# Kernel optimization log

Measured on AMD Instinct MI355X. Metric: run time of the kernel, lower is better.

The kernel has to match this reference:

```python
import jax, jax.numpy as jnp
import numpy as np

N_HEADS = 16
NEG_INF = -1e9


def setup_inputs() -> dict:
    key = jax.random.key(0)
    ks = jax.random.split(key, 8)
    B, S, D = 2, 2048, 1024
    HD = D // N_HEADS
    x = jax.random.normal(ks[0], (B, S, D), dtype=jnp.float32)
    # RoPE frequencies (llama-style): theta = 10000^(-2i/head_dim)
    inv_freq = 1.0 / (10000.0 ** (np.arange(0, HD, 2, dtype=np.float32) / HD))  # [HD//2]
    angles = np.arange(S, dtype=np.float32)[:, None] * inv_freq[None, :]        # [S, HD//2]
    freqs_cos = jnp.asarray(np.cos(angles))
    freqs_sin = jnp.asarray(np.sin(angles))
    # additive causal mask [1,1,S,S]
    mask = jnp.where(np.tril(np.ones((S, S), dtype=bool)), 0.0, NEG_INF).astype(jnp.float32)[None, None]
    scale = 0.02
    wq = jax.random.normal(ks[1], (D, D), dtype=jnp.float32) * scale
    wk = jax.random.normal(ks[2], (D, D), dtype=jnp.float32) * scale
    wv = jax.random.normal(ks[3], (D, D), dtype=jnp.float32) * scale
    wo = jax.random.normal(ks[4], (D, D), dtype=jnp.float32) * scale
    return {"x": x, "freqs_cos": freqs_cos, "freqs_sin": freqs_sin, "mask": mask,
            "wq": wq, "wk": wk, "wv": wv, "wo": wo}


def _rope(t, cos, sin):
    # t: [B,S,H,HD]; cos/sin: [S,HD//2]; complex mult (t0 + i t1) * (cos + i sin)
    b, s, h, hd = t.shape
    tr = t.reshape(b, s, h, hd // 2, 2)
    t0, t1 = tr[..., 0], tr[..., 1]
    c = cos[None, :, None, :]
    sn = sin[None, :, None, :]
    out = jnp.stack([t0 * c - t1 * sn, t0 * sn + t1 * c], axis=-1)
    return out.reshape(b, s, h, hd)


def reference(x, freqs_cos, freqs_sin, mask, wq, wk, wv, wo):
    b, s, d = x.shape
    hd = d // N_HEADS
    # torch Linear: y = x @ W.T
    xq = (x @ wq.T).reshape(b, s, N_HEADS, hd)
    xk = (x @ wk.T).reshape(b, s, N_HEADS, hd)
    xv = (x @ wv.T).reshape(b, s, N_HEADS, hd)
    xq = _rope(xq, freqs_cos, freqs_sin)
    xk = _rope(xk, freqs_cos, freqs_sin)
    # [B,H,S,S] scores
    scores = jnp.einsum('bqhd,bkhd->bhqk', xq, xk) / jnp.sqrt(jnp.asarray(hd, x.dtype))
    scores = scores + mask
    probs = jax.nn.softmax(scores.astype(jnp.float32), axis=-1).astype(x.dtype)
    out = jnp.einsum('bhqk,bkhd->bqhd', probs, xv).reshape(b, s, d)
    return out @ wo.T
```

## Files before the change

kernel.cpp:

```cpp
#include <hip/hip_runtime.h>
#include <hip/hip_bf16.h>
#include <cstdint>

typedef __attribute__((ext_vector_type(4))) float f32x4;
typedef __attribute__((ext_vector_type(8))) short s16x8;
typedef __attribute__((ext_vector_type(4))) unsigned short u16x4;
typedef unsigned short u16;
typedef unsigned int u32;
typedef unsigned long long u64;

__device__ __forceinline__ float b2f(u16 u){ u32 v = ((u32)u)<<16; return __builtin_bit_cast(float, v); }
__device__ __forceinline__ u16 f2b(float f){
  __hip_bfloat16 h = __float2bfloat16(f);
  return __builtin_bit_cast(u16, h);
}

__device__ __forceinline__ void gld16(const void* g, void* l){
  __builtin_amdgcn_global_load_lds((const __attribute__((address_space(1))) void*)g,
                                   (__attribute__((address_space(3))) void*)l, 16, 0, 0);
}

__device__ __forceinline__ f32x4 mfma16(s16x8 a, s16x8 b, f32x4 c){
  return __builtin_amdgcn_mfma_f32_16x16x32_bf16(a, b, c, 0, 0, 0);
}

#define WS_XB   0u
#define WS_WQ   (4u<<20)
#define WS_WK   (5u<<20)
#define WS_WV   (6u<<20)
#define WS_WO   (7u<<20)
#define WS_Q    (8u<<20)
#define WS_K    (12u<<20)
#define WS_VT   (16u<<20)
#define WS_AO   (20u<<20)

#define QSCALE 0.18033688f

__global__ __launch_bounds__(256) void k_convert(const float* __restrict__ x,
    const float* __restrict__ wq, const float* __restrict__ wk,
    const float* __restrict__ wv, const float* __restrict__ wo,
    u16* __restrict__ ws){
  u32 idx = blockIdx.x*256u + threadIdx.x;
  const float* src; u16* dst;
  if (idx < (1u<<20)) { src = x + (u64)idx*4u; dst = ws + WS_XB + (u64)idx*4u; }
  else {
    u32 widx = idx - (1u<<20);
    u32 wsel = widx >> 18;
    u32 off  = (widx & ((1u<<18)-1u)) * 4u;
    const float* sp = (wsel==0u)?wq:(wsel==1u)?wk:(wsel==2u)?wv:wo;
    src = sp + off; dst = ws + WS_WQ + (u64)wsel*(1u<<20) + off;
  }
  f32x4 v = *(const f32x4*)src;
  u16x4 o = { f2b(v[0]), f2b(v[1]), f2b(v[2]), f2b(v[3]) };
  *(u16x4*)dst = o;
}

__global__ __launch_bounds__(256,2) void k_gemm(u16* __restrict__ ws, float* __restrict__ out,
    const float* __restrict__ fc, const float* __restrict__ fs, int pass){
  __shared__ char sm[65536];
  const u32 tid = threadIdx.x;
  const u32 w = tid>>6, l = tid&63u, g = l>>4, li = l&15u;
  const u32 wr = w>>1, wc = w&1u;
  u32 bx = blockIdx.x;

  const u16 *Ap, *Bp; u32 arow0, brow0; int mode;
  if (pass == 0) {
    u32 seg = bx >> 8, b2 = bx & 255u;
    if (seg < 2u) {
      Ap = ws + WS_XB; Bp = ws + (seg ? WS_WK : WS_WQ);
      arow0 = (b2 >> 3) * 128u; brow0 = (b2 & 7u) * 128u; mode = (int)seg;
    } else {
      Ap = ws + WS_WV; Bp = ws + WS_XB;
      arow0 = (b2 >> 5) * 128u; brow0 = (b2 & 31u) * 128u; mode = 2;
    }
  } else {
    Ap = ws + WS_AO; Bp = ws + WS_WO;
    arow0 = (bx >> 3) * 128u; brow0 = (bx & 7u) * 128u; mode = 3;
  }

  f32x4 acc[4][4];
  #pragma unroll
  for (u32 m=0;m<4;++m)
    #pragma unroll
    for (u32 n=0;n<4;++n) acc[m][n] = 0.0f;

  auto STAGE_G = [&](u32 s, u32 t){
    const u32 k0 = t*64u;
    #pragma unroll
    for (u32 j = 0; j < 4u; ++j) {
      u32 p = w*4096u + j*1024u + l*16u;
      u32 row = p >> 7, colb = p & 127u;
      u32 cS = colb ^ ((row & 7u) << 4);
      gld16(Ap + (u64)(arow0 + row)*1024u + k0 + (cS>>1), sm + s*32768u + w*4096u + j*1024u);
      gld16(Bp + (u64)(brow0 + row)*1024u + k0 + (cS>>1), sm + s*32768u + 16384u + w*4096u + j*1024u);
    }
  };

  STAGE_G(0u, 0u);
  __syncthreads();

  u32 cur = 0u;
  for (u32 t = 0; t < 16u; ++t) {
    if (t + 1u < 16u) STAGE_G(cur^1u, t+1u);
    const u32 cb = cur*32768u;
    s16x8 af[2][4], bf[2][4];
    #pragma unroll
    for (u32 kk=0;kk<2u;++kk){
      #pragma unroll
      for (u32 m=0;m<4;++m){
        u32 row = wr*64u + m*16u + li;
        af[kk][m] = *(const s16x8*)(sm + cb + row*128u + ((kk*64u + g*16u) ^ ((row&7u)<<4)));
      }
      #pragma unroll
      for (u32 n=0;n<4;++n){
        u32 row = wc*64u + n*16u + li;
        bf[kk][n] = *(const s16x8*)(sm + cb + 16384u + row*128u + ((kk*64u + g*16u) ^ ((row&7u)<<4)));
      }
    }
    #pragma unroll
    for (u32 kk=0;kk<2u;++kk)
      #pragma unroll
      for (u32 m=0;m<4;++m)
        #pragma unroll
        for (u32 n=0;n<4;++n)
          acc[m][n] = mfma16(af[kk][m], bf[kk][n], acc[m][n]);
    __syncthreads();
    cur ^= 1u;
  }

  u16* qdst = ws + WS_Q; u16* kdst = ws + WS_K; u16* vtd = ws + WS_VT;
  if (mode <= 1) {
    #pragma unroll
    for (u32 m=0;m<4;++m)
      #pragma unroll
      for (u32 n=0;n<4;++n)
        #pragma unroll
        for (u32 q=0;q<4;++q){
          u32 row = wr*64u + m*16u + 4u*g + q;
          u32 colb = (wc*64u + n*16u + li)*2u;
          *(u16*)(sm + row*256u + (colb ^ ((row&7u)<<4))) = f2b(acc[m][n][q]);
        }
    __syncthreads();
    u32 row = tid >> 1, half = tid & 1u;
    u32 r = arow0 + row;
    u32 b = r >> 11, s = r & 2047u;
    u32 h = (brow0 >> 6) + half;
    float qs = (mode==0) ? QSCALE : 1.0f;
    u16* d = ((mode==0) ? qdst : kdst) + (u64)(((b<<4)+h)*2048u + s)*64u;
    #pragma unroll
    for (u32 u0=0; u0<8u; ++u0){
      s16x8 cv = *(const s16x8*)(sm + row*256u + ((half*128u + u0*16u) ^ ((row&7u)<<4)));
      f32x4 cvv = *(const f32x4*)(fc + s*32u + u0*4u);
      f32x4 svv = *(const f32x4*)(fs + s*32u + u0*4u);
      s16x8 o;
      #pragma unroll
      for (u32 i=0;i<4;++i){
        float t0 = b2f((u16)cv[2*i]), t1 = b2f((u16)cv[2*i+1]);
        o[2*i]   = (short)f2b((t0*cvv[i] - t1*svv[i])*qs);
        o[2*i+1] = (short)f2b((t0*svv[i] + t1*cvv[i])*qs);
      }
      *(s16x8*)(d + u0*8u) = o;
    }
  } else {
    #pragma unroll
    for (u32 m=0;m<4;++m){
      u32 r0 = arow0 + wr*64u + m*16u + 4u*g;
      #pragma unroll
      for (u32 n=0;n<4;++n){
        u32 c = brow0 + wc*64u + n*16u + li;
        #pragma unroll
        for (u32 q=0;q<4;++q){
          float v = acc[m][n][q];
          u32 r = r0 + q;
          if (mode == 2) vtd[(u64)r*4096u + c] = f2b(v);
          else           out[(u64)r*1024u + c] = v;
        }
      }
    }
  }
}

__global__ __launch_bounds__(256) void k_attn(u16* __restrict__ ws){
  __shared__ char sm[41984];
  const u32 tid = threadIdx.x;
  const u32 w = tid>>6, l = tid&63u, g = l>>4, li = l&15u;
  u32 bx = blockIdx.x;
  u32 qt = 31u - (bx >> 5);
  u32 bh = bx & 31u;
  u32 b = bh >> 4, h = bh & 15u;
  const u16* Q  = ws + WS_Q + (u64)bh*2048u*64u;
  const u16* Kp = ws + WS_K + (u64)bh*2048u*64u;
  const u16* Vt = ws + WS_VT + (u64)(h*64u)*4096u + b*2048u;
  u16* AO = ws + WS_AO;
  const u32 qw = qt*64u + w*16u;

  s16x8 qa[2];
  #pragma unroll
  for (u32 kk=0;kk<2;++kk)
    qa[kk] = *(const s16x8*)(Q + (u64)(qw + li)*64u + kk*32u + g*8u);

  s16x8 ones;
  #pragma unroll
  for (u32 i=0;i<8;++i) ones[i] = (short)0x3F80;

  f32x4 o[4]; f32x4 lsum;
  #pragma unroll
  for (u32 n=0;n<4;++n) o[n] = 0.0f;
  lsum = 0.0f;

  char* pl = sm + 32768 + w*2304u;
  const u32 nt = qt + 1u;

  auto STAGE = [&](u32 s, u32 kvb){
    #pragma unroll
    for (u32 j=0;j<2u;++j){
      u32 p = (w*2u+j)*1024u + l*16u;
      u32 row = p >> 7, colb = p & 127u;
      u32 cS = colb ^ ((row & 7u) << 4);
      gld16(Kp + (u64)(kvb + row)*64u + (cS>>1), sm + s*16384u + (w*2u+j)*1024u);
      gld16(Vt + (u64)row*4096u + kvb + (cS>>1), sm + s*16384u + 8192u + (w*2u+j)*1024u);
    }
  };

  STAGE(0u, 0u);
  __syncthreads();

  u32 cur = 0u;
  for (u32 t = 0; t < nt; ++t) {
    const u32 kvb = t*64u;
    if (t + 1u < nt) STAGE(cur^1u, kvb + 64u);
    const u32 cb = cur*16384u;

    f32x4 sv[4];
    #pragma unroll
    for (u32 n=0;n<4;++n) sv[n] = 0.0f;
    #pragma unroll
    for (u32 n=0;n<4;++n){
      u32 kvr = n*16u + li;
      #pragma unroll
      for (u32 kk=0;kk<2u;++kk){
        s16x8 kf = *(const s16x8*)(sm + cb + kvr*128u + ((kk*64u + g*16u) ^ ((kvr&7u)<<4)));
        sv[n] = mfma16(qa[kk], kf, sv[n]);
      }
    }
    if (t == nt - 1u) {
      #pragma unroll
      for (u32 n=0;n<4;++n)
        #pragma unroll
        for (u32 q=0;q<4;++q){
          u32 qr = qw + 4u*g + q;
          u32 kc = kvb + n*16u + li;
          if (kc > qr) sv[n][q] = -1e9f;
        }
    }
    #pragma unroll
    for (u32 n=0;n<4;++n)
      #pragma unroll
      for (u32 q=0;q<4;++q)
        *(u16*)(pl + (4u*g + q)*144u + (n*16u + li)*2u) = f2b(exp2f(sv[n][q]));
    #pragma unroll
    for (u32 kk=0;kk<2u;++kk){
      s16x8 pa = *(const s16x8*)(pl + li*144u + kk*64u + g*16u);
      lsum = mfma16(pa, ones, lsum);
      #pragma unroll
      for (u32 n=0;n<4;++n){
        u32 hr = n*16u + li;
        s16x8 vf = *(const s16x8*)(sm + cb + 8192u + hr*128u + ((kk*64u + g*16u) ^ ((hr&7u)<<4)));
        o[n] = mfma16(pa, vf, o[n]);
      }
    }
    __syncthreads();
    cur ^= 1u;
  }

  #pragma unroll
  for (u32 q=0;q<4;++q){
    float inv = 1.0f / lsum[q];
    u32 qr = qw + 4u*g + q;
    #pragma unroll
    for (u32 n=0;n<4;++n){
      u32 hd = n*16u + li;
      AO[((u64)(b*2048u + qr))*1024u + h*64u + hd] = f2b(o[n][q] * inv);
    }
  }
}

extern "C" void kernel_launch(void* const* d_in, const int* in_sizes, int n_in,
                              void* d_out, int out_size, void* d_ws, size_t ws_size,
                              hipStream_t stream) {
  const float* x  = (const float*)d_in[0];
  const float* fc = (const float*)d_in[1];
  const float* fs = (const float*)d_in[2];
  const float* wq = (const float*)d_in[4];
  const float* wk = (const float*)d_in[5];
  const float* wv = (const float*)d_in[6];
  const float* wo = (const float*)d_in[7];
  u16* ws = (u16*)d_ws;
  float* out = (float*)d_out;

  k_convert<<<8192, 256, 0, stream>>>(x, wq, wk, wv, wo, ws);
  k_gemm  <<<768,  256, 0, stream>>>(ws, out, fc, fs, 0);
  k_attn  <<<1024, 256, 0, stream>>>(ws);
  k_gemm  <<<256,  256, 0, stream>>>(ws, out, fc, fs, 1);
}
```

Measured before the change: 108.3 us.

## Rewrite attention as single-wave 32x32 MFMA kernel with register-only P exchange

The attention kernel now runs as one 64-lane wave per 32-query tile instead of a 4-wave block per 64 queries. It uses 32x32x16 bf16 MFMA and computes S^T = K·Q^T so that the probability fragments can be rearranged with cross-half lane shuffles rather than a round trip through LDS. K and V are loaded straight from global memory into registers each iteration; the LDS double-buffering and the __syncthreads barriers are removed. This trades shared-memory staging and reuse across waves for more global/L2 traffic and higher register pressure, in exchange for removing LDS round trips and block-level synchronization.

New measurement: 139.1 us. 28.4% more time.

```diff
diff --git a/kernel.cpp b/kernel.cpp
--- a/kernel.cpp
+++ b/kernel.cpp
@@ -3,8 +3,10 @@
 #include <cstdint>
 
 typedef __attribute__((ext_vector_type(4))) float f32x4;
+typedef __attribute__((ext_vector_type(16))) float f32x16;
 typedef __attribute__((ext_vector_type(8))) short s16x8;
 typedef __attribute__((ext_vector_type(4))) unsigned short u16x4;
+typedef __attribute__((ext_vector_type(4))) unsigned int u32x4;
 typedef unsigned short u16;
 typedef unsigned int u32;
 typedef unsigned long long u64;
@@ -22,6 +24,9 @@
 
 __device__ __forceinline__ f32x4 mfma16(s16x8 a, s16x8 b, f32x4 c){
   return __builtin_amdgcn_mfma_f32_16x16x32_bf16(a, b, c, 0, 0, 0);
+}
+__device__ __forceinline__ f32x16 mfma32(s16x8 a, s16x8 b, f32x16 c){
+  return __builtin_amdgcn_mfma_f32_32x32x16_bf16(a, b, c, 0, 0, 0);
 }
 
 #define WS_XB   0u
@@ -180,108 +185,95 @@
   }
 }
 
-__global__ __launch_bounds__(256) void k_attn(u16* __restrict__ ws){
-  __shared__ char sm[41984];
-  const u32 tid = threadIdx.x;
-  const u32 w = tid>>6, l = tid&63u, g = l>>4, li = l&15u;
-  u32 bx = blockIdx.x;
-  u32 qt = 31u - (bx >> 5);
-  u32 bh = bx & 31u;
-  u32 b = bh >> 4, h = bh & 15u;
+__global__ __launch_bounds__(64) void k_attn(u16* __restrict__ ws){
+  const u32 lane = threadIdx.x & 63u;
+  const u32 q = lane & 31u, h = lane >> 5;
+  const bool lo = lane < 32u;
+  u32 u = blockIdx.x;
+  u32 qs = 63u - (u >> 5);
+  u32 bh = u & 31u;
+  u32 b = bh >> 4, head = bh & 15u;
   const u16* Q  = ws + WS_Q + (u64)bh*2048u*64u;
   const u16* Kp = ws + WS_K + (u64)bh*2048u*64u;
-  const u16* Vt = ws + WS_VT + (u64)(h*64u)*4096u + b*2048u;
+  const u16* Vt = ws + WS_VT + (u64)(head*64u)*4096u + b*2048u;
   u16* AO = ws + WS_AO;
-  const u32 qw = qt*64u + w*16u;
-
-  s16x8 qa[2];
-  #pragma unroll
-  for (u32 kk=0;kk<2;++kk)
-    qa[kk] = *(const s16x8*)(Q + (u64)(qw + li)*64u + kk*32u + g*8u);
+
+  s16x8 qf[4];
+  #pragma unroll
+  for (u32 kk=0;kk<4;++kk)
+    qf[kk] = *(const s16x8*)(Q + (u64)(qs*32u + q)*64u + kk*16u + h*8u);
 
   s16x8 ones;
   #pragma unroll
   for (u32 i=0;i<8;++i) ones[i] = (short)0x3F80;
 
-  f32x4 o[4]; f32x4 lsum;
-  #pragma unroll
-  for (u32 n=0;n<4;++n) o[n] = 0.0f;
-  lsum = 0.0f;
-
-  char* pl = sm + 32768 + w*2304u;
-  const u32 nt = qt + 1u;
-
-  auto STAGE = [&](u32 s, u32 kvb){
-    #pragma unroll
-    for (u32 j=0;j<2u;++j){
-      u32 p = (w*2u+j)*1024u + l*16u;
-      u32 row = p >> 7, colb = p & 127u;
-      u32 cS = colb ^ ((row & 7u) << 4);
-      gld16(Kp + (u64)(kvb + row)*64u + (cS>>1), sm + s*16384u + (w*2u+j)*1024u);
-      gld16(Vt + (u64)row*4096u + kvb + (cS>>1), sm + s*16384u + 8192u + (w*2u+j)*1024u);
-    }
-  };
-
-  STAGE(0u, 0u);
-  __syncthreads();
-
-  u32 cur = 0u;
+  f32x16 o0, o1, lsum;
+  #pragma unroll
+  for (u32 r=0;r<16;++r){ o0[r]=0.0f; o1[r]=0.0f; lsum[r]=0.0f; }
+
+  const u32 qg = qs*32u + q;
+  const u32 nt = (qs >> 1) + 1u;
   for (u32 t = 0; t < nt; ++t) {
     const u32 kvb = t*64u;
-    if (t + 1u < nt) STAGE(cur^1u, kvb + 64u);
-    const u32 cb = cur*16384u;
-
-    f32x4 sv[4];
-    #pragma unroll
-    for (u32 n=0;n<4;++n) sv[n] = 0.0f;
-    #pragma unroll
-    for (u32 n=0;n<4;++n){
-      u32 kvr = n*16u + li;
-      #pragma unroll
-      for (u32 kk=0;kk<2u;++kk){
-        s16x8 kf = *(const s16x8*)(sm + cb + kvr*128u + ((kk*64u + g*16u) ^ ((kvr&7u)<<4)));
-        sv[n] = mfma16(qa[kk], kf, sv[n]);
-      }
+    s16x8 vf[8];
+    #pragma unroll
+    for (u32 d=0; d<2u; ++d)
+      #pragma unroll
+      for (u32 ks=0; ks<4u; ++ks)
+        vf[d*4u+ks] = *(const s16x8*)(Vt + (u64)(d*32u + q)*4096u + kvb + ks*16u + h*8u);
+    s16x8 kf[8];
+    #pragma unroll
+    for (u32 s=0; s<2u; ++s)
+      #pragma unroll
+      for (u32 kk=0; kk<4u; ++kk)
+        kf[s*4u+kk] = *(const s16x8*)(Kp + (u64)(kvb + s*32u + q)*64u + kk*16u + h*8u);
+
+    f32x16 sv0, sv1;
+    #pragma unroll
+    for (u32 r=0;r<16;++r){ sv0[r]=0.0f; sv1[r]=0.0f; }
+    #pragma unroll
+    for (u32 kk=0;kk<4u;++kk){
+      sv0 = mfma32(kf[kk],     qf[kk], sv0);
+      sv1 = mfma32(kf[4u+kk],  qf[kk], sv1);
     }
     if (t == nt - 1u) {
       #pragma unroll
-      for (u32 n=0;n<4;++n)
-        #pragma unroll
-        for (u32 q=0;q<4;++q){
-          u32 qr = qw + 4u*g + q;
-          u32 kc = kvb + n*16u + li;
-          if (kc > qr) sv[n][q] = -1e9f;
-        }
-    }
-    #pragma unroll
-    for (u32 n=0;n<4;++n)
-      #pragma unroll
-      for (u32 q=0;q<4;++q)
-        *(u16*)(pl + (4u*g + q)*144u + (n*16u + li)*2u) = f2b(exp2f(sv[n][q]));
-    #pragma unroll
-    for (u32 kk=0;kk<2u;++kk){
-      s16x8 pa = *(const s16x8*)(pl + li*144u + kk*64u + g*16u);
-      lsum = mfma16(pa, ones, lsum);
-      #pragma unroll
-      for (u32 n=0;n<4;++n){
-        u32 hr = n*16u + li;
-        s16x8 vf = *(const s16x8*)(sm + cb + 8192u + hr*128u + ((kk*64u + g*16u) ^ ((hr&7u)<<4)));
-        o[n] = mfma16(pa, vf, o[n]);
-      }
-    }
-    __syncthreads();
-    cur ^= 1u;
-  }
-
-  #pragma unroll
-  for (u32 q=0;q<4;++q){
-    float inv = 1.0f / lsum[q];
-    u32 qr = qw + 4u*g + q;
-    #pragma unroll
-    for (u32 n=0;n<4;++n){
-      u32 hd = n*16u + li;
-      AO[((u64)(b*2048u + qr))*1024u + h*64u + hd] = f2b(o[n][q] * inv);
-    }
+      for (u32 r=0;r<16;++r){
+        u32 kv0 = kvb + (r&3u) + 8u*(r>>2) + 4u*h;
+        if (kv0       > qg) sv0[r] = -1e9f;
+        if (kv0 + 32u > qg) sv1[r] = -1e9f;
+      }
+    }
+    #pragma unroll
+    for (u32 r=0;r<16;++r){ sv0[r] = exp2f(sv0[r]); sv1[r] = exp2f(sv1[r]); }
+    u32 a[16];
+    #pragma unroll
+    for (u32 j=0;j<8u;++j){
+      asm("v_cvt_pk_bf16_f32 %0, %1, %2" : "=v"(a[j])    : "v"(sv0[2u*j]), "v"(sv0[2u*j+1u]));
+      asm("v_cvt_pk_bf16_f32 %0, %1, %2" : "=v"(a[8u+j]) : "v"(sv1[2u*j]), "v"(sv1[2u*j+1u]));
+    }
+    #pragma unroll
+    for (u32 ks=0; ks<4u; ++ks){
+      u32 b0 = ks*4u;
+      u32 x0 = a[b0], x1 = a[b0+1u], y0 = a[b0+2u], y1 = a[b0+3u];
+      u32 y0s = __shfl_xor(y0, 32), y1s = __shfl_xor(y1, 32);
+      u32 x0s = __shfl_xor(x0, 32), x1s = __shfl_xor(x1, 32);
+      u32x4 paw = { lo ? x0 : y0s,  lo ? x1 : y1s,
+                    lo ? x0s : y0,  lo ? x1s : y1 };
+      s16x8 pa = __builtin_bit_cast(s16x8, paw);
+      lsum = mfma32(pa, ones, lsum);
+      o0 = mfma32(pa, vf[ks],     o0);
+      o1 = mfma32(pa, vf[4u+ks],  o1);
+    }
+  }
+
+  #pragma unroll
+  for (u32 r=0;r<16;++r){
+    float inv = 1.0f / lsum[r];
+    u32 row = b*2048u + qs*32u + (r&3u) + 8u*(r>>2) + 4u*h;
+    u64 base = (u64)row*1024u + head*64u + q;
+    AO[base]       = f2b(o0[r] * inv);
+    AO[base + 32u] = f2b(o1[r] * inv);
   }
 }
 
@@ -300,6 +292,6 @@
 
   k_convert<<<8192, 256, 0, stream>>>(x, wq, wk, wv, wo, ws);
   k_gemm  <<<768,  256, 0, stream>>>(ws, out, fc, fs, 0);
-  k_attn  <<<1024, 256, 0, stream>>>(ws);
+  k_attn  <<<2048, 64,  0, stream>>>(ws);
   k_gemm  <<<256,  256, 0, stream>>>(ws, out, fc, fs, 1);
 }
```
